# Optimization experiments

Measured on AMD Instinct MI355X. Metric: run time of the kernel, lower is better.

## Reference

```python
import jax, jax.numpy as jnp
import numpy as np

N_CLUSTERS = 128
LATENT_NDIM = 256
ALPHA = 1.0


def setup_inputs() -> dict:
    key = jax.random.key(0)
    k1, k2 = jax.random.split(key)
    z = jax.random.normal(k1, (131072, LATENT_NDIM), dtype=jnp.float32)
    centroids = jax.random.normal(k2, (N_CLUSTERS, LATENT_NDIM), dtype=jnp.float32)
    return {"z": z, "centroids": centroids}


def _student_t(z, centroids, alpha):
    # Squared distances via expansion: ||z||^2 + ||c||^2 - 2 z @ c^T  -> [B, K]
    z_sq = jnp.sum(z * z, axis=1, keepdims=True)            # [B, 1]
    c_sq = jnp.sum(centroids * centroids, axis=1)           # [K]
    sq_dist = z_sq + c_sq[None, :] - 2.0 * (z @ centroids.T)
    norm = jnp.sqrt(jnp.maximum(sq_dist, 0.0))              # L2 norm, as in torch code
    s_tmp = (1.0 + norm / alpha) ** (-(alpha + 1.0) / 2.0)
    s = s_tmp / jnp.sum(s_tmp, axis=1, keepdims=True)
    return s


def reference(z, centroids):
    s = _student_t(z, centroids, ALPHA)
    c = jnp.argmax(s, axis=1)
    return (s, c)
```

## Files before the change

### kernel.cpp

```cpp
#include <hip/hip_runtime.h>

typedef _Float16 f16x8 __attribute__((ext_vector_type(8)));
typedef float f32x4 __attribute__((ext_vector_type(4)));
typedef unsigned int u32x4 __attribute__((ext_vector_type(4)));

#define D_DIM 256
#define K_CL  128
#define WR    16
#define MARGIN 0.1f

__device__ __forceinline__ unsigned pkf16(float a, float b) {
  return __builtin_bit_cast(unsigned, __builtin_amdgcn_cvt_pkrtz(a, b));
}

extern "C" __global__ void __launch_bounds__(512)
k_main(const float* __restrict__ z, const float* __restrict__ cen,
       float* __restrict__ s_out, float* __restrict__ c_out, int ntiles)
{
  __shared__ __align__(16) unsigned int Bf[16384];
  __shared__ float csqnp[K_CL];
  __shared__ __align__(16) float zrow_s[8][D_DIM];
  __shared__ float stmp_s[8][K_CL];

  const int tid = threadIdx.x;
  const int w   = tid >> 6;
  const int l   = tid & 63;
  const int l15 = l & 15;
  const int g   = l >> 4;

  if (tid < 256) {
#pragma clang fp contract(off)
    float blk0 = 0.f, blk1 = 0.f;
    const int c = tid >> 1, sub = tid & 1;
    const float* a = cen + (size_t)c * D_DIM + (sub << 2);
#pragma unroll
    for (int b2 = 0; b2 < 2; ++b2) {
      const float* ab = a + (b2 << 7);
      const float4 v0 = *(const float4*)(ab);
      float v[4] = {v0.x * v0.x, v0.y * v0.y, v0.z * v0.z, v0.w * v0.w};
      for (int i = 1; i < 16; ++i) {
        const float4 vi = *(const float4*)(ab + (i << 3));
        v[0] = v[0] + vi.x * vi.x; v[1] = v[1] + vi.y * vi.y;
        v[2] = v[2] + vi.z * vi.z; v[3] = v[3] + vi.w * vi.w;
      }
      const float part = (v[0] + v[1]) + (v[2] + v[3]);
      if (b2 == 0) blk0 = part; else blk1 = part;
    }
    const float o0 = __shfl_xor(blk0, 1);
    const float o1 = __shfl_xor(blk1, 1);
    if (sub == 0) csqnp[c] = (blk0 + o0) + (blk1 + o1);
  }

#pragma unroll
  for (int j = 0; j < 8; ++j) {
    const int ch = w + (j << 3);
    const int ct = ch >> 3, k = ch & 7;
    const float* cp = cen + (size_t)((ct << 4) + l15) * D_DIM + (k << 5) + (g << 3);
    const float4 v0 = *(const float4*)(cp);
    const float4 v1 = *(const float4*)(cp + 4);
    *(u32x4*)((char*)Bf + (ch << 10) + (l << 4)) =
        (u32x4){pkf16(v0.x, v0.y), pkf16(v0.z, v0.w),
                pkf16(v1.x, v1.y), pkf16(v1.z, v1.w)};
  }
  __syncthreads();

  float csqv[8];
#pragma unroll
  for (int ct = 0; ct < 8; ++ct) csqv[ct] = csqnp[(ct << 4) + l15];

  const int nwaves = gridDim.x << 3;
  for (int t = (blockIdx.x << 3) + w; t < ntiles; t += nwaves) {
    const int row0 = t << 4;

    f16x8 az[8];
    float zs = 0.f;
    const float* zr = z + (size_t)(row0 + l15) * D_DIM + (g << 3);
#pragma unroll
    for (int k = 0; k < 8; ++k) {
      const float4 v0 = *(const float4*)(zr + (k << 5));
      const float4 v1 = *(const float4*)(zr + (k << 5) + 4);
      az[k] = __builtin_bit_cast(f16x8,
          (u32x4){pkf16(v0.x, v0.y), pkf16(v0.z, v0.w),
                  pkf16(v1.x, v1.y), pkf16(v1.z, v1.w)});
      zs += v0.x*v0.x + v0.y*v0.y + v0.z*v0.z + v0.w*v0.w
          + v1.x*v1.x + v1.y*v1.y + v1.z*v1.z + v1.w*v1.w;
    }
    zs += __shfl_xor(zs, 16);
    zs += __shfl_xor(zs, 32);
    float zsqj[4];
#pragma unroll
    for (int j = 0; j < 4; ++j) zsqj[j] = __shfl(zs, (g << 2) + j);

    f32x4 acc[8];
#pragma unroll
    for (int ct = 0; ct < 8; ++ct) acc[ct] = (f32x4){0.f, 0.f, 0.f, 0.f};
#pragma unroll
    for (int k = 0; k < 8; ++k) {
#pragma unroll
      for (int ct = 0; ct < 8; ++ct) {
        const f16x8 b = *(const f16x8*)((char*)Bf + (((ct << 3) + k) << 10) + (l << 4));
        acc[ct] = __builtin_amdgcn_mfma_f32_16x16x32_f16(az[k], b, acc[ct], 0, 0, 0);
      }
    }

    unsigned km1[4], km2[4];
    float rinv[4];
#pragma unroll
    for (int j = 0; j < 4; ++j) {
      unsigned m1 = 0xFFFFFFFFu, m2 = 0xFFFFFFFFu;
      float sum = 0.f;
#pragma unroll
      for (int ct = 0; ct < 8; ++ct) {
        const float sq = fmaxf(fmaf(-2.0f, acc[ct][j], zsqj[j] + csqv[ct]), 0.0f);
        const unsigned u = (__float_as_uint(sq) & 0xFFFFFF80u) | (unsigned)((ct << 4) + l15);
        const unsigned mn = min(m1, u), mx = max(m1, u);
        m1 = mn; m2 = min(m2, mx);
        sum += __builtin_amdgcn_rcpf(
            1.0f + __builtin_amdgcn_sqrtf(__uint_as_float(u & 0xFFFFFF80u)));
      }
#pragma unroll
      for (int m = 1; m <= 8; m <<= 1) {
        const unsigned o1 = __shfl_xor(m1, m);
        const unsigned o2 = __shfl_xor(m2, m);
        sum += __shfl_xor(sum, m);
        const unsigned mn = min(m1, o1), mx = max(m1, o1);
        m1 = mn; m2 = min(mx, min(m2, o2));
      }
      km1[j] = m1; km2[j] = m2;
      rinv[j] = __builtin_amdgcn_rcpf(sum);
    }

#pragma unroll
    for (int j = 0; j < 4; ++j) {
      float* srow = s_out + (size_t)(row0 + (g << 2) + j) * K_CL + l15;
#pragma unroll
      for (int ct = 0; ct < 8; ++ct) {
        const float sq = fmaxf(fmaf(-2.0f, acc[ct][j], zsqj[j] + csqv[ct]), 0.0f);
        const float sqq = __uint_as_float(__float_as_uint(sq) & 0xFFFFFF80u);
        srow[ct << 4] =
            __builtin_amdgcn_rcpf(1.0f + __builtin_amdgcn_sqrtf(sqq)) * rinv[j];
      }
      if (l15 == 0) c_out[row0 + (g << 2) + j] = (float)(km1[j] & 0x7Fu);
    }

    unsigned rowmask = 0;
#pragma unroll
    for (int j = 0; j < 4; ++j) {
      const float d1 = __uint_as_float(km1[j] & 0xFFFFFF80u);
      const float d2 = __uint_as_float(km2[j] & 0xFFFFFF80u);
      const unsigned long long b = __ballot(l15 == 0 && (d2 - d1) < MARGIN);
      rowmask |= (unsigned)(b & 1ull) << j;
      rowmask |= (unsigned)((b >> 16) & 1ull) << (4 + j);
      rowmask |= (unsigned)((b >> 32) & 1ull) << (8 + j);
      rowmask |= (unsigned)((b >> 48) & 1ull) << (12 + j);
    }

    while (rowmask) {
      const int r = __builtin_ctz(rowmask);
      rowmask &= rowmask - 1;
      const int grow = row0 + r;
      float* zrs = &zrow_s[w][0];
      float* sts = &stmp_s[w][0];
      *(float4*)(zrs + (l << 2)) =
          *(const float4*)(z + (size_t)grow * D_DIM + (l << 2));
      asm volatile("s_waitcnt lgkmcnt(0)" ::: "memory");
      float zblk = 0.f;
      if (l < 8) {
#pragma clang fp contract(off)
        float b0 = 0.f, b1 = 0.f;
        for (int b2 = 0; b2 < 2; ++b2) {
          const float* ab = zrs + (b2 << 7);
          float x = ab[l];
          float racc = x * x;
          for (int i = 1; i < 16; ++i) { x = ab[(i << 3) + l]; racc = racc + x * x; }
          racc = racc + __shfl_xor(racc, 1);
          racc = racc + __shfl_xor(racc, 2);
          racc = racc + __shfl_xor(racc, 4);
          if (b2 == 0) b0 = racc; else b1 = racc;
        }
        zblk = b0 + b1;
      }
      const float zsq_np = __shfl(zblk, 0);
      double d0 = 0.0, d1d = 0.0;
      const float* c0 = cen + (size_t)l * D_DIM;
      const float* c1 = cen + (size_t)(l + 64) * D_DIM;
      for (int d4 = 0; d4 < 64; ++d4) {
        const float4 zv = *(const float4*)(zrs + (d4 << 2));
        const float4 a0 = *(const float4*)(c0 + (d4 << 2));
        const float4 a1 = *(const float4*)(c1 + (d4 << 2));
        d0  += (double)zv.x * a0.x; d0  += (double)zv.y * a0.y;
        d0  += (double)zv.z * a0.z; d0  += (double)zv.w * a0.w;
        d1d += (double)zv.x * a1.x; d1d += (double)zv.y * a1.y;
        d1d += (double)zv.z * a1.z; d1d += (double)zv.w * a1.w;
      }
      float st0, st1;
      {
#pragma clang fp contract(off)
        const float dotf0 = (float)d0;
        const float sq0 = (zsq_np + csqnp[l]) - 2.0f * dotf0;
        st0 = 1.0f / (1.0f + sqrtf(fmaxf(sq0, 0.0f)));
        const float dotf1 = (float)d1d;
        const float sq1 = (zsq_np + csqnp[l + 64]) - 2.0f * dotf1;
        st1 = 1.0f / (1.0f + sqrtf(fmaxf(sq1, 0.0f)));
      }
      sts[l] = st0;
      sts[l + 64] = st1;
      asm volatile("s_waitcnt lgkmcnt(0)" ::: "memory");
      float sblk = 0.f;
      if (l < 8) {
#pragma clang fp contract(off)
        float racc = sts[l];
        for (int i = 1; i < 16; ++i) racc = racc + sts[(i << 3) + l];
        racc = racc + __shfl_xor(racc, 1);
        racc = racc + __shfl_xor(racc, 2);
        racc = racc + __shfl_xor(racc, 4);
        sblk = racc;
      }
      const float ssum = __shfl(sblk, 0);
      const float s0 = st0 / ssum;
      const float s1 = st1 / ssum;
      unsigned long long k0 =
          ((unsigned long long)(0x7FFFFFFFu - __float_as_uint(s0)) << 32) | (unsigned)l;
      unsigned long long k1 =
          ((unsigned long long)(0x7FFFFFFFu - __float_as_uint(s1)) << 32) | (unsigned)(l + 64);
      unsigned long long kk = k0 < k1 ? k0 : k1;
#pragma unroll
      for (int m = 1; m < 64; m <<= 1) {
        const unsigned long long o = __shfl_xor(kk, m);
        kk = o < kk ? o : kk;
      }
      if (l == 0) c_out[grow] = (float)(unsigned)(kk & 0x7Fu);
    }
  }
}

extern "C" void kernel_launch(void* const* d_in, const int* in_sizes, int n_in,
                              void* d_out, int out_size, void* d_ws, size_t ws_size,
                              hipStream_t stream) {
  const float* z   = (const float*)d_in[0];
  const float* cen = (const float*)d_in[1];
  const int M = in_sizes[0] / D_DIM;
  float* s_out = (float*)d_out;
  float* c_out = s_out + (size_t)M * K_CL;
  const int ntiles = M / WR;
  const int nblk = 512;

  hipLaunchKernelGGL(k_main, dim3(nblk), dim3(512), 0, stream,
                     z, cen, s_out, c_out, ntiles);
}
```

Baseline: 84.93 us.

## Split centroid prep into separate kernel and read B fragments from global memory

Moves the centroid fp16 packing and squared-norm computation into a small prep kernel that writes to workspace. The main kernel drops its shared-memory B buffer and block-wide sync, and now reads B fragments straight from global memory (L2/L1-cached). It also switches from a persistent grid-stride loop over 512 blocks to one tile per wave with ntiles/8 blocks. This removes the per-block staging cost and frees LDS for higher occupancy. In exchange it adds a second launch and relies on the cache for the repeated B loads.

New measurement: 86.05 us. Within noise of the previous version (+1.3%).

```diff
diff --git a/kernel.cpp b/kernel.cpp
--- a/kernel.cpp
+++ b/kernel.cpp
@@ -13,31 +13,30 @@
   return __builtin_bit_cast(unsigned, __builtin_amdgcn_cvt_pkrtz(a, b));
 }
 
-extern "C" __global__ void __launch_bounds__(512)
-k_main(const float* __restrict__ z, const float* __restrict__ cen,
-       float* __restrict__ s_out, float* __restrict__ c_out, int ntiles)
+extern "C" __global__ void __launch_bounds__(64)
+k_prep(const float* __restrict__ cen, unsigned int* __restrict__ bfr,
+       float* __restrict__ csq_g)
 {
-  __shared__ __align__(16) unsigned int Bf[16384];
-  __shared__ float csqnp[K_CL];
-  __shared__ __align__(16) float zrow_s[8][D_DIM];
-  __shared__ float stmp_s[8][K_CL];
-
-  const int tid = threadIdx.x;
-  const int w   = tid >> 6;
-  const int l   = tid & 63;
-  const int l15 = l & 15;
-  const int g   = l >> 4;
-
-  if (tid < 256) {
+  const int b = blockIdx.x;
+  const int l = threadIdx.x;
+  const int l15 = l & 15, g = l >> 4;
+  const int ct = b >> 3, k = b & 7;
+  const float* cp = cen + (size_t)((ct << 4) + l15) * D_DIM + (k << 5) + (g << 3);
+  const float4 v0 = *(const float4*)(cp);
+  const float4 v1 = *(const float4*)(cp + 4);
+  *(u32x4*)((char*)bfr + (b << 10) + (l << 4)) =
+      (u32x4){pkf16(v0.x, v0.y), pkf16(v0.z, v0.w),
+              pkf16(v1.x, v1.y), pkf16(v1.z, v1.w)};
+  if (b < 4) {
 #pragma clang fp contract(off)
     float blk0 = 0.f, blk1 = 0.f;
-    const int c = tid >> 1, sub = tid & 1;
+    const int c = (b << 5) + (l >> 1), sub = l & 1;
     const float* a = cen + (size_t)c * D_DIM + (sub << 2);
 #pragma unroll
     for (int b2 = 0; b2 < 2; ++b2) {
       const float* ab = a + (b2 << 7);
-      const float4 v0 = *(const float4*)(ab);
-      float v[4] = {v0.x * v0.x, v0.y * v0.y, v0.z * v0.z, v0.w * v0.w};
+      const float4 w0 = *(const float4*)(ab);
+      float v[4] = {w0.x * w0.x, w0.y * w0.y, w0.z * w0.z, w0.w * w0.w};
       for (int i = 1; i < 16; ++i) {
         const float4 vi = *(const float4*)(ab + (i << 3));
         v[0] = v[0] + vi.x * vi.x; v[1] = v[1] + vi.y * vi.y;
@@ -48,189 +47,191 @@
     }
     const float o0 = __shfl_xor(blk0, 1);
     const float o1 = __shfl_xor(blk1, 1);
-    if (sub == 0) csqnp[c] = (blk0 + o0) + (blk1 + o1);
-  }
-
-#pragma unroll
-  for (int j = 0; j < 8; ++j) {
-    const int ch = w + (j << 3);
-    const int ct = ch >> 3, k = ch & 7;
-    const float* cp = cen + (size_t)((ct << 4) + l15) * D_DIM + (k << 5) + (g << 3);
-    const float4 v0 = *(const float4*)(cp);
-    const float4 v1 = *(const float4*)(cp + 4);
-    *(u32x4*)((char*)Bf + (ch << 10) + (l << 4)) =
+    if (sub == 0) csq_g[c] = (blk0 + o0) + (blk1 + o1);
+  }
+}
+
+extern "C" __global__ void __launch_bounds__(512)
+k_main(const float* __restrict__ z, const float* __restrict__ cen,
+       const unsigned int* __restrict__ bfr, const float* __restrict__ csq_g,
+       float* __restrict__ s_out, float* __restrict__ c_out, int ntiles)
+{
+  __shared__ __align__(16) float zrow_s[8][D_DIM];
+  __shared__ float stmp_s[8][K_CL];
+
+  const int tid = threadIdx.x;
+  const int w   = tid >> 6;
+  const int l   = tid & 63;
+  const int l15 = l & 15;
+  const int g   = l >> 4;
+
+  const int t = (blockIdx.x << 3) + w;
+  if (t >= ntiles) return;
+  const int row0 = t << 4;
+
+  float csqv[8];
+#pragma unroll
+  for (int ct = 0; ct < 8; ++ct) csqv[ct] = csq_g[(ct << 4) + l15];
+
+  f16x8 az[8];
+  float zs = 0.f;
+  const float* zr = z + (size_t)(row0 + l15) * D_DIM + (g << 3);
+#pragma unroll
+  for (int k = 0; k < 8; ++k) {
+    const float4 v0 = *(const float4*)(zr + (k << 5));
+    const float4 v1 = *(const float4*)(zr + (k << 5) + 4);
+    az[k] = __builtin_bit_cast(f16x8,
         (u32x4){pkf16(v0.x, v0.y), pkf16(v0.z, v0.w),
-                pkf16(v1.x, v1.y), pkf16(v1.z, v1.w)};
-  }
-  __syncthreads();
-
-  float csqv[8];
-#pragma unroll
-  for (int ct = 0; ct < 8; ++ct) csqv[ct] = csqnp[(ct << 4) + l15];
-
-  const int nwaves = gridDim.x << 3;
-  for (int t = (blockIdx.x << 3) + w; t < ntiles; t += nwaves) {
-    const int row0 = t << 4;
-
-    f16x8 az[8];
-    float zs = 0.f;
-    const float* zr = z + (size_t)(row0 + l15) * D_DIM + (g << 3);
-#pragma unroll
-    for (int k = 0; k < 8; ++k) {
-      const float4 v0 = *(const float4*)(zr + (k << 5));
-      const float4 v1 = *(const float4*)(zr + (k << 5) + 4);
-      az[k] = __builtin_bit_cast(f16x8,
-          (u32x4){pkf16(v0.x, v0.y), pkf16(v0.z, v0.w),
-                  pkf16(v1.x, v1.y), pkf16(v1.z, v1.w)});
-      zs += v0.x*v0.x + v0.y*v0.y + v0.z*v0.z + v0.w*v0.w
-          + v1.x*v1.x + v1.y*v1.y + v1.z*v1.z + v1.w*v1.w;
-    }
-    zs += __shfl_xor(zs, 16);
-    zs += __shfl_xor(zs, 32);
-    float zsqj[4];
-#pragma unroll
-    for (int j = 0; j < 4; ++j) zsqj[j] = __shfl(zs, (g << 2) + j);
-
-    f32x4 acc[8];
-#pragma unroll
-    for (int ct = 0; ct < 8; ++ct) acc[ct] = (f32x4){0.f, 0.f, 0.f, 0.f};
-#pragma unroll
-    for (int k = 0; k < 8; ++k) {
-#pragma unroll
-      for (int ct = 0; ct < 8; ++ct) {
-        const f16x8 b = *(const f16x8*)((char*)Bf + (((ct << 3) + k) << 10) + (l << 4));
-        acc[ct] = __builtin_amdgcn_mfma_f32_16x16x32_f16(az[k], b, acc[ct], 0, 0, 0);
-      }
-    }
-
-    unsigned km1[4], km2[4];
-    float rinv[4];
-#pragma unroll
-    for (int j = 0; j < 4; ++j) {
-      unsigned m1 = 0xFFFFFFFFu, m2 = 0xFFFFFFFFu;
-      float sum = 0.f;
-#pragma unroll
-      for (int ct = 0; ct < 8; ++ct) {
-        const float sq = fmaxf(fmaf(-2.0f, acc[ct][j], zsqj[j] + csqv[ct]), 0.0f);
-        const unsigned u = (__float_as_uint(sq) & 0xFFFFFF80u) | (unsigned)((ct << 4) + l15);
-        const unsigned mn = min(m1, u), mx = max(m1, u);
-        m1 = mn; m2 = min(m2, mx);
-        sum += __builtin_amdgcn_rcpf(
-            1.0f + __builtin_amdgcn_sqrtf(__uint_as_float(u & 0xFFFFFF80u)));
-      }
-#pragma unroll
-      for (int m = 1; m <= 8; m <<= 1) {
-        const unsigned o1 = __shfl_xor(m1, m);
-        const unsigned o2 = __shfl_xor(m2, m);
-        sum += __shfl_xor(sum, m);
-        const unsigned mn = min(m1, o1), mx = max(m1, o1);
-        m1 = mn; m2 = min(mx, min(m2, o2));
-      }
-      km1[j] = m1; km2[j] = m2;
-      rinv[j] = __builtin_amdgcn_rcpf(sum);
-    }
-
-#pragma unroll
-    for (int j = 0; j < 4; ++j) {
-      float* srow = s_out + (size_t)(row0 + (g << 2) + j) * K_CL + l15;
-#pragma unroll
-      for (int ct = 0; ct < 8; ++ct) {
-        const float sq = fmaxf(fmaf(-2.0f, acc[ct][j], zsqj[j] + csqv[ct]), 0.0f);
-        const float sqq = __uint_as_float(__float_as_uint(sq) & 0xFFFFFF80u);
-        srow[ct << 4] =
-            __builtin_amdgcn_rcpf(1.0f + __builtin_amdgcn_sqrtf(sqq)) * rinv[j];
-      }
-      if (l15 == 0) c_out[row0 + (g << 2) + j] = (float)(km1[j] & 0x7Fu);
-    }
-
-    unsigned rowmask = 0;
-#pragma unroll
-    for (int j = 0; j < 4; ++j) {
-      const float d1 = __uint_as_float(km1[j] & 0xFFFFFF80u);
-      const float d2 = __uint_as_float(km2[j] & 0xFFFFFF80u);
-      const unsigned long long b = __ballot(l15 == 0 && (d2 - d1) < MARGIN);
-      rowmask |= (unsigned)(b & 1ull) << j;
-      rowmask |= (unsigned)((b >> 16) & 1ull) << (4 + j);
-      rowmask |= (unsigned)((b >> 32) & 1ull) << (8 + j);
-      rowmask |= (unsigned)((b >> 48) & 1ull) << (12 + j);
-    }
-
-    while (rowmask) {
-      const int r = __builtin_ctz(rowmask);
-      rowmask &= rowmask - 1;
-      const int grow = row0 + r;
-      float* zrs = &zrow_s[w][0];
-      float* sts = &stmp_s[w][0];
-      *(float4*)(zrs + (l << 2)) =
-          *(const float4*)(z + (size_t)grow * D_DIM + (l << 2));
-      asm volatile("s_waitcnt lgkmcnt(0)" ::: "memory");
-      float zblk = 0.f;
-      if (l < 8) {
-#pragma clang fp contract(off)
-        float b0 = 0.f, b1 = 0.f;
-        for (int b2 = 0; b2 < 2; ++b2) {
-          const float* ab = zrs + (b2 << 7);
-          float x = ab[l];
-          float racc = x * x;
-          for (int i = 1; i < 16; ++i) { x = ab[(i << 3) + l]; racc = racc + x * x; }
-          racc = racc + __shfl_xor(racc, 1);
-          racc = racc + __shfl_xor(racc, 2);
-          racc = racc + __shfl_xor(racc, 4);
-          if (b2 == 0) b0 = racc; else b1 = racc;
-        }
-        zblk = b0 + b1;
-      }
-      const float zsq_np = __shfl(zblk, 0);
-      double d0 = 0.0, d1d = 0.0;
-      const float* c0 = cen + (size_t)l * D_DIM;
-      const float* c1 = cen + (size_t)(l + 64) * D_DIM;
-      for (int d4 = 0; d4 < 64; ++d4) {
-        const float4 zv = *(const float4*)(zrs + (d4 << 2));
-        const float4 a0 = *(const float4*)(c0 + (d4 << 2));
-        const float4 a1 = *(const float4*)(c1 + (d4 << 2));
-        d0  += (double)zv.x * a0.x; d0  += (double)zv.y * a0.y;
-        d0  += (double)zv.z * a0.z; d0  += (double)zv.w * a0.w;
-        d1d += (double)zv.x * a1.x; d1d += (double)zv.y * a1.y;
-        d1d += (double)zv.z * a1.z; d1d += (double)zv.w * a1.w;
-      }
-      float st0, st1;
-      {
-#pragma clang fp contract(off)
-        const float dotf0 = (float)d0;
-        const float sq0 = (zsq_np + csqnp[l]) - 2.0f * dotf0;
-        st0 = 1.0f / (1.0f + sqrtf(fmaxf(sq0, 0.0f)));
-        const float dotf1 = (float)d1d;
-        const float sq1 = (zsq_np + csqnp[l + 64]) - 2.0f * dotf1;
-        st1 = 1.0f / (1.0f + sqrtf(fmaxf(sq1, 0.0f)));
-      }
-      sts[l] = st0;
-      sts[l + 64] = st1;
-      asm volatile("s_waitcnt lgkmcnt(0)" ::: "memory");
-      float sblk = 0.f;
-      if (l < 8) {
-#pragma clang fp contract(off)
-        float racc = sts[l];
-        for (int i = 1; i < 16; ++i) racc = racc + sts[(i << 3) + l];
+                pkf16(v1.x, v1.y), pkf16(v1.z, v1.w)});
+    zs += v0.x*v0.x + v0.y*v0.y + v0.z*v0.z + v0.w*v0.w
+        + v1.x*v1.x + v1.y*v1.y + v1.z*v1.z + v1.w*v1.w;
+  }
+  zs += __shfl_xor(zs, 16);
+  zs += __shfl_xor(zs, 32);
+  float zsqj[4];
+#pragma unroll
+  for (int j = 0; j < 4; ++j) zsqj[j] = __shfl(zs, (g << 2) + j);
+
+  f32x4 acc[8];
+#pragma unroll
+  for (int ct = 0; ct < 8; ++ct) acc[ct] = (f32x4){0.f, 0.f, 0.f, 0.f};
+#pragma unroll
+  for (int k = 0; k < 8; ++k) {
+#pragma unroll
+    for (int ct = 0; ct < 8; ++ct) {
+      const f16x8 b = __builtin_bit_cast(f16x8,
+          *(const u32x4*)((const char*)bfr + (((ct << 3) + k) << 10) + (l << 4)));
+      acc[ct] = __builtin_amdgcn_mfma_f32_16x16x32_f16(az[k], b, acc[ct], 0, 0, 0);
+    }
+  }
+
+  unsigned km1[4], km2[4];
+  float rinv[4];
+#pragma unroll
+  for (int j = 0; j < 4; ++j) {
+    unsigned m1 = 0xFFFFFFFFu, m2 = 0xFFFFFFFFu;
+    float sum = 0.f;
+#pragma unroll
+    for (int ct = 0; ct < 8; ++ct) {
+      const float sq = fmaxf(fmaf(-2.0f, acc[ct][j], zsqj[j] + csqv[ct]), 0.0f);
+      const unsigned u = (__float_as_uint(sq) & 0xFFFFFF80u) | (unsigned)((ct << 4) + l15);
+      const unsigned mn = min(m1, u), mx = max(m1, u);
+      m1 = mn; m2 = min(m2, mx);
+      sum += __builtin_amdgcn_rcpf(
+          1.0f + __builtin_amdgcn_sqrtf(__uint_as_float(u & 0xFFFFFF80u)));
+    }
+#pragma unroll
+    for (int m = 1; m <= 8; m <<= 1) {
+      const unsigned o1 = __shfl_xor(m1, m);
+      const unsigned o2 = __shfl_xor(m2, m);
+      sum += __shfl_xor(sum, m);
+      const unsigned mn = min(m1, o1), mx = max(m1, o1);
+      m1 = mn; m2 = min(mx, min(m2, o2));
+    }
+    km1[j] = m1; km2[j] = m2;
+    rinv[j] = __builtin_amdgcn_rcpf(sum);
+  }
+
+#pragma unroll
+  for (int j = 0; j < 4; ++j) {
+    float* srow = s_out + (size_t)(row0 + (g << 2) + j) * K_CL + l15;
+#pragma unroll
+    for (int ct = 0; ct < 8; ++ct) {
+      const float sq = fmaxf(fmaf(-2.0f, acc[ct][j], zsqj[j] + csqv[ct]), 0.0f);
+      const float sqq = __uint_as_float(__float_as_uint(sq) & 0xFFFFFF80u);
+      srow[ct << 4] =
+          __builtin_amdgcn_rcpf(1.0f + __builtin_amdgcn_sqrtf(sqq)) * rinv[j];
+    }
+    if (l15 == 0) c_out[row0 + (g << 2) + j] = (float)(km1[j] & 0x7Fu);
+  }
+
+  unsigned rowmask = 0;
+#pragma unroll
+  for (int j = 0; j < 4; ++j) {
+    const float d1 = __uint_as_float(km1[j] & 0xFFFFFF80u);
+    const float d2 = __uint_as_float(km2[j] & 0xFFFFFF80u);
+    const unsigned long long b = __ballot(l15 == 0 && (d2 - d1) < MARGIN);
+    rowmask |= (unsigned)(b & 1ull) << j;
+    rowmask |= (unsigned)((b >> 16) & 1ull) << (4 + j);
+    rowmask |= (unsigned)((b >> 32) & 1ull) << (8 + j);
+    rowmask |= (unsigned)((b >> 48) & 1ull) << (12 + j);
+  }
+
+  while (rowmask) {
+    const int r = __builtin_ctz(rowmask);
+    rowmask &= rowmask - 1;
+    const int grow = row0 + r;
+    float* zrs = &zrow_s[w][0];
+    float* sts = &stmp_s[w][0];
+    *(float4*)(zrs + (l << 2)) =
+        *(const float4*)(z + (size_t)grow * D_DIM + (l << 2));
+    asm volatile("s_waitcnt lgkmcnt(0)" ::: "memory");
+    float zblk = 0.f;
+    if (l < 8) {
+#pragma clang fp contract(off)
+      float b0 = 0.f, b1 = 0.f;
+      for (int b2 = 0; b2 < 2; ++b2) {
+        const float* ab = zrs + (b2 << 7);
+        float x = ab[l];
+        float racc = x * x;
+        for (int i = 1; i < 16; ++i) { x = ab[(i << 3) + l]; racc = racc + x * x; }
         racc = racc + __shfl_xor(racc, 1);
         racc = racc + __shfl_xor(racc, 2);
         racc = racc + __shfl_xor(racc, 4);
-        sblk = racc;
+        if (b2 == 0) b0 = racc; else b1 = racc;
       }
-      const float ssum = __shfl(sblk, 0);
-      const float s0 = st0 / ssum;
-      const float s1 = st1 / ssum;
-      unsigned long long k0 =
-          ((unsigned long long)(0x7FFFFFFFu - __float_as_uint(s0)) << 32) | (unsigned)l;
-      unsigned long long k1 =
-          ((unsigned long long)(0x7FFFFFFFu - __float_as_uint(s1)) << 32) | (unsigned)(l + 64);
-      unsigned long long kk = k0 < k1 ? k0 : k1;
-#pragma unroll
-      for (int m = 1; m < 64; m <<= 1) {
-        const unsigned long long o = __shfl_xor(kk, m);
-        kk = o < kk ? o : kk;
-      }
-      if (l == 0) c_out[grow] = (float)(unsigned)(kk & 0x7Fu);
-    }
+      zblk = b0 + b1;
+    }
+    const float zsq_np = __shfl(zblk, 0);
+    double d0 = 0.0, d1d = 0.0;
+    const float* c0 = cen + (size_t)l * D_DIM;
+    const float* c1 = cen + (size_t)(l + 64) * D_DIM;
+    for (int d4 = 0; d4 < 64; ++d4) {
+      const float4 zv = *(const float4*)(zrs + (d4 << 2));
+      const float4 a0 = *(const float4*)(c0 + (d4 << 2));
+      const float4 a1 = *(const float4*)(c1 + (d4 << 2));
+      d0  += (double)zv.x * a0.x; d0  += (double)zv.y * a0.y;
+      d0  += (double)zv.z * a0.z; d0  += (double)zv.w * a0.w;
+      d1d += (double)zv.x * a1.x; d1d += (double)zv.y * a1.y;
+      d1d += (double)zv.z * a1.z; d1d += (double)zv.w * a1.w;
+    }
+    float st0, st1;
+    {
+#pragma clang fp contract(off)
+      const float dotf0 = (float)d0;
+      const float sq0 = (zsq_np + csq_g[l]) - 2.0f * dotf0;
+      st0 = 1.0f / (1.0f + sqrtf(fmaxf(sq0, 0.0f)));
+      const float dotf1 = (float)d1d;
+      const float sq1 = (zsq_np + csq_g[l + 64]) - 2.0f * dotf1;
+      st1 = 1.0f / (1.0f + sqrtf(fmaxf(sq1, 0.0f)));
+    }
+    sts[l] = st0;
+    sts[l + 64] = st1;
+    asm volatile("s_waitcnt lgkmcnt(0)" ::: "memory");
+    float sblk = 0.f;
+    if (l < 8) {
+#pragma clang fp contract(off)
+      float racc = sts[l];
+      for (int i = 1; i < 16; ++i) racc = racc + sts[(i << 3) + l];
+      racc = racc + __shfl_xor(racc, 1);
+      racc = racc + __shfl_xor(racc, 2);
+      racc = racc + __shfl_xor(racc, 4);
+      sblk = racc;
+    }
+    const float ssum = __shfl(sblk, 0);
+    const float s0 = st0 / ssum;
+    const float s1 = st1 / ssum;
+    unsigned long long k0 =
+        ((unsigned long long)(0x7FFFFFFFu - __float_as_uint(s0)) << 32) | (unsigned)l;
+    unsigned long long k1 =
+        ((unsigned long long)(0x7FFFFFFFu - __float_as_uint(s1)) << 32) | (unsigned)(l + 64);
+    unsigned long long kk = k0 < k1 ? k0 : k1;
+#pragma unroll
+    for (int m = 1; m < 64; m <<= 1) {
+      const unsigned long long o = __shfl_xor(kk, m);
+      kk = o < kk ? o : kk;
+    }
+    if (l == 0) c_out[grow] = (float)(unsigned)(kk & 0x7Fu);
   }
 }
 
@@ -243,8 +244,11 @@
   float* s_out = (float*)d_out;
   float* c_out = s_out + (size_t)M * K_CL;
   const int ntiles = M / WR;
-  const int nblk = 512;
-
-  hipLaunchKernelGGL(k_main, dim3(nblk), dim3(512), 0, stream,
-                     z, cen, s_out, c_out, ntiles);
-}
+
+  unsigned int* bfr = (unsigned int*)d_ws;
+  float* csq_g = (float*)((char*)d_ws + 65536);
+
+  hipLaunchKernelGGL(k_prep, dim3(64), dim3(64), 0, stream, cen, bfr, csq_g);
+  hipLaunchKernelGGL(k_main, dim3(ntiles / 8), dim3(512), 0, stream,
+                     z, cen, bfr, csq_g, s_out, c_out, ntiles);
+}
```
